# Kernel optimization log

Measured on AMD Instinct MI355X. Metric: run time of the kernel, lower is better.

## Reference

```python
import jax, jax.numpy as jnp
import numpy as np

HEADS = 8
DIM_HEAD = 64
QUERY_DIM = 1024
CONTEXT_DIM = 768
INNER = HEADS * DIM_HEAD  # 512


def setup_inputs() -> dict:
    key = jax.random.key(0)
    ks = jax.random.split(key, 8)
    b, n, j = 4, 2048, 2048
    x = jax.random.normal(ks[0], (b, n, QUERY_DIM), dtype=jnp.float32)
    context = jax.random.normal(ks[1], (b, j, CONTEXT_DIM), dtype=jnp.float32)
    mask = jax.random.randint(ks[2], (b, j), 0, 2).astype(jnp.bool_)
    # weights stored as (in, out) so forward is x @ W (torch Linear stores transpose)
    W_q = jax.random.normal(ks[3], (QUERY_DIM, INNER), dtype=jnp.float32) / np.sqrt(QUERY_DIM)
    W_k = jax.random.normal(ks[4], (CONTEXT_DIM, INNER), dtype=jnp.float32) / np.sqrt(CONTEXT_DIM)
    W_v = jax.random.normal(ks[5], (CONTEXT_DIM, INNER), dtype=jnp.float32) / np.sqrt(CONTEXT_DIM)
    W_o = jax.random.normal(ks[6], (INNER, QUERY_DIM), dtype=jnp.float32) / np.sqrt(INNER)
    b_o = jax.random.normal(ks[7], (QUERY_DIM,), dtype=jnp.float32) * 0.01
    return {"x": x, "context": context, "mask": mask,
            "W_q": W_q, "W_k": W_k, "W_v": W_v, "W_o": W_o, "b_o": b_o}


def reference(x, context, mask, W_q, W_k, W_v, W_o, b_o):
    b, n, _ = x.shape
    j = context.shape[1]
    scale = DIM_HEAD ** -0.5
    # projections -> [b, n, h, d]
    q = (x @ W_q).reshape(b, n, HEADS, DIM_HEAD)
    k = (context @ W_k).reshape(b, j, HEADS, DIM_HEAD)
    v = (context @ W_v).reshape(b, j, HEADS, DIM_HEAD)
    # similarity [b, h, n, j]
    sim = jnp.einsum('bihd,bjhd->bhij', q, k) * scale
    max_neg = -jnp.finfo(sim.dtype).max
    sim = jnp.where(mask[:, None, None, :], sim, max_neg)
    attn = jax.nn.softmax(sim, axis=-1)
    out = jnp.einsum('bhij,bjhd->bihd', attn, v).reshape(b, n, INNER)
    return out @ W_o + b_o  # dropout is identity (p=0 / eval)
```

## Files before the change

kernel.cpp:

```cpp
#include <hip/hip_runtime.h>
#include <hip/hip_bf16.h>

typedef __attribute__((ext_vector_type(4)))  float  f32x4;
typedef __attribute__((ext_vector_type(16))) float  f32x16;
typedef __attribute__((ext_vector_type(8)))  short  bf16x8;
typedef __attribute__((ext_vector_type(4)))  int    int32x4;
typedef __attribute__((ext_vector_type(2)))  unsigned int uint32x2;

#define DEVINL static __device__ __forceinline__
#define GAS __attribute__((address_space(1)))
#define LAS __attribute__((address_space(3)))

DEVINL ushort f2bf(float f) {
  unsigned u = __builtin_bit_cast(unsigned, f);
  unsigned r = u + 0x7fffu + ((u >> 16) & 1u);
  return (ushort)(r >> 16);
}

DEVINL unsigned cvtpk(float lo, float hi) {
  unsigned r;
  asm("v_cvt_pk_bf16_f32 %0, %1, %2" : "=v"(r) : "v"(lo), "v"(hi));
  return r;
}

DEVINL void plswap(unsigned &a, unsigned &b) {
  asm("v_permlane32_swap_b32 %0, %1" : "+v"(a), "+v"(b));
}

DEVINL float fexp2(float x) { return __builtin_amdgcn_exp2f(x); }

DEVINL float bf2f(short s) {
  return __builtin_bit_cast(float, ((unsigned)(ushort)s) << 16);
}

DEVINL f32x4 mfma16(bf16x8 a, bf16x8 b, f32x4 c) {
  return __builtin_amdgcn_mfma_f32_16x16x32_bf16(a, b, c, 0, 0, 0);
}
DEVINL f32x16 mfma32(bf16x8 a, bf16x8 b, f32x16 c) {
  return __builtin_amdgcn_mfma_f32_32x32x16_bf16(a, b, c, 0, 0, 0);
}

__global__ __launch_bounds__(256)
void prep_k(const int* __restrict__ msk, float* __restrict__ mbias,
            const float* __restrict__ Wq, const float* __restrict__ Wk,
            const float* __restrict__ Wv, const float* __restrict__ Wo,
            ushort* __restrict__ WqT, ushort* __restrict__ WkT,
            ushort* __restrict__ WvT, ushort* __restrict__ WoT)
{
  __shared__ ushort Ts[64][72];
  int id = blockIdx.x;
  if (id >= 448) {
    int tid = (id - 448) * 256 + threadIdx.x;
    if (tid < 8192) mbias[tid] = msk[tid] ? 0.f : -1e30f;
    return;
  }
  const float* src; ushort* dst; int Kd, Nd, lid;
  if (id < 128)      { src = Wq; dst = WqT; Kd = 1024; Nd = 512;  lid = id; }
  else if (id < 224) { src = Wk; dst = WkT; Kd = 768;  Nd = 512;  lid = id - 128; }
  else if (id < 320) { src = Wv; dst = WvT; Kd = 768;  Nd = 512;  lid = id - 224; }
  else               { src = Wo; dst = WoT; Kd = 512;  Nd = 1024; lid = id - 320; }
  const int sh = (Nd == 512) ? 3 : 4;
  const int kb = lid >> sh, nb = lid & ((1 << sh) - 1);
  const int k0 = kb * 64, n0 = nb * 64;
  const int t = threadIdx.x;
  const int r = t >> 2, c0 = (t & 3) * 16;

  const float* sp = src + (size_t)(k0 + r) * Nd + n0 + c0;
  f32x4 v0 = *(const f32x4*)(sp);
  f32x4 v1 = *(const f32x4*)(sp + 4);
  f32x4 v2 = *(const f32x4*)(sp + 8);
  f32x4 v3 = *(const f32x4*)(sp + 12);
  #pragma unroll
  for (int e = 0; e < 4; e++) {
    Ts[c0 + e][r]      = f2bf(v0[e]);
    Ts[c0 + 4 + e][r]  = f2bf(v1[e]);
    Ts[c0 + 8 + e][r]  = f2bf(v2[e]);
    Ts[c0 + 12 + e][r] = f2bf(v3[e]);
  }
  __syncthreads();
  const int n = t >> 2, kc = (t & 3) * 16;
  bf16x8 o0 = *(const bf16x8*)&Ts[n][kc];
  bf16x8 o1 = *(const bf16x8*)&Ts[n][kc + 8];
  ushort* dp = dst + (size_t)(n0 + n) * Kd + k0 + kc;
  *(bf16x8*)dp       = o0;
  *(bf16x8*)(dp + 8) = o1;
}

template<int PHASE>
__global__ __launch_bounds__(256)
void mm_k(const float* __restrict__ xf, const float* __restrict__ cf,
          const ushort* __restrict__ WqT, const ushort* __restrict__ WkT,
          const ushort* __restrict__ WvT,
          ushort* __restrict__ Qb, ushort* __restrict__ Kb, ushort* __restrict__ VT,
          const ushort* __restrict__ AO, const ushort* __restrict__ WoT,
          float* __restrict__ out, const float* __restrict__ bias)
{
  constexpr int AST = (PHASE == 0) ? 40 : 32;
  __shared__ ushort As[2][128 * AST];
  __shared__ ushort Bs[2][128 * 32];

  const float* Af = nullptr; const ushort* Ab = nullptr; const ushort* BT;
  ushort* Cw = nullptr;
  int Kd, mode, m0, n0;
  if (PHASE == 0) {
    int id = blockIdx.x;
    id = (id & 7) * 96 + (id >> 3);
    const int which = id >> 8, local = id & 255;
    m0 = (local >> 2) * 128; n0 = (local & 3) * 128;
    if (which == 0)      { Af = xf; BT = WqT; Cw = Qb; Kd = 1024; mode = 1; }
    else if (which == 1) { Af = cf; BT = WkT; Cw = Kb; Kd = 768;  mode = 1; }
    else                 { Af = cf; BT = WvT; Cw = VT; Kd = 768;  mode = 2; }
  } else {
    int id = blockIdx.x;
    id = (id & 7) * 64 + (id >> 3);
    m0 = (id >> 3) * 128; n0 = (id & 7) * 128;
    Ab = AO; BT = WoT; Kd = 512; mode = 0;
  }

  const int t = threadIdx.x, lane = t & 63, w = t >> 6;
  const int wr = w >> 1, wc = w & 1;
  const int g = lane >> 4, ql = lane & 15;

  const int arow = t >> 1, akc = (t & 1) * 16;
  const int srowo = 16 * w + (lane >> 2);
  const int sgg = (lane & 3) ^ ((lane >> 3) & 3);

  f32x4 acc[4][4];
  #pragma unroll
  for (int i = 0; i < 4; i++)
    #pragma unroll
    for (int j = 0; j < 4; j++) acc[i][j] = (f32x4){0.f, 0.f, 0.f, 0.f};

  auto stageB = [&](int buf, int k0) {
    #pragma unroll
    for (int i = 0; i < 2; i++) {
      const int row = i * 64 + srowo;
      const ushort* bsrc = BT + (size_t)(n0 + row) * Kd + k0 + sgg * 8;
      __builtin_amdgcn_global_load_lds((const GAS void*)bsrc,
          (LAS void*)&Bs[buf][(i * 64 + 16 * w) * 32], 16, 0, 0);
    }
  };
  auto stageA_lds = [&](int buf, int k0) {
    #pragma unroll
    for (int i = 0; i < 2; i++) {
      const int row = i * 64 + srowo;
      const ushort* asrc = Ab + (size_t)(m0 + row) * Kd + k0 + sgg * 8;
      __builtin_amdgcn_global_load_lds((const GAS void*)asrc,
          (LAS void*)&As[buf][(i * 64 + 16 * w) * 32], 16, 0, 0);
    }
  };
  auto writeA_f32 = [&](int buf, const f32x4& v0, const f32x4& v1,
                        const f32x4& v2, const f32x4& v3) {
    union { unsigned u[4]; int32x4 v; } w1_, w2_;
    w1_.u[0] = cvtpk(v0[0], v0[1]); w1_.u[1] = cvtpk(v0[2], v0[3]);
    w1_.u[2] = cvtpk(v1[0], v1[1]); w1_.u[3] = cvtpk(v1[2], v1[3]);
    w2_.u[0] = cvtpk(v2[0], v2[1]); w2_.u[1] = cvtpk(v2[2], v2[3]);
    w2_.u[2] = cvtpk(v3[0], v3[1]); w2_.u[3] = cvtpk(v3[2], v3[3]);
    ushort* dst = &As[buf][arow * 40 + akc];
    *(int32x4*)dst       = w1_.v;
    *(int32x4*)(dst + 8) = w2_.v;
  };

  const int NK = Kd >> 5;
  if (PHASE == 0) {
    const float* ap = Af + (size_t)(m0 + arow) * Kd + akc;
    f32x4 v0 = *(const f32x4*)(ap);
    f32x4 v1 = *(const f32x4*)(ap + 4);
    f32x4 v2 = *(const f32x4*)(ap + 8);
    f32x4 v3 = *(const f32x4*)(ap + 12);
    writeA_f32(0, v0, v1, v2, v3);
    stageB(0, 0);
  } else {
    stageA_lds(0, 0);
    stageB(0, 0);
  }
  __syncthreads();

  const int sel = (ql >> 1) & 3;
  const int koff = (g ^ sel) * 8;

  for (int tt = 0; tt < NK; tt++) {
    const int cur = tt & 1;
    const bool pre = (tt + 1 < NK);

    f32x4 n0v, n1v, n2v, n3v;
    if (PHASE == 0) {
      if (pre) {
        const float* ap = Af + (size_t)(m0 + arow) * Kd + (tt + 1) * 32 + akc;
        n0v = *(const f32x4*)(ap);
        n1v = *(const f32x4*)(ap + 4);
        n2v = *(const f32x4*)(ap + 8);
        n3v = *(const f32x4*)(ap + 12);
        stageB(cur ^ 1, (tt + 1) * 32);
      }
    } else {
      if (pre) { stageA_lds(cur ^ 1, (tt + 1) * 32); stageB(cur ^ 1, (tt + 1) * 32); }
    }

    bf16x8 af[4], bfr[4];
    #pragma unroll
    for (int i = 0; i < 4; i++) {
      if (PHASE == 0)
        af[i] = *(const bf16x8*)&As[cur][(wr * 64 + i * 16 + ql) * 40 + g * 8];
      else
        af[i] = *(const bf16x8*)&As[cur][(wr * 64 + i * 16 + ql) * 32 + koff];
      bfr[i] = *(const bf16x8*)&Bs[cur][(wc * 64 + i * 16 + ql) * 32 + koff];
    }
    #pragma unroll
    for (int i = 0; i < 4; i++)
      #pragma unroll
      for (int j = 0; j < 4; j++)
        acc[i][j] = mfma16(af[i], bfr[j], acc[i][j]);

    if (PHASE == 0 && pre) writeA_f32(cur ^ 1, n0v, n1v, n2v, n3v);
    __syncthreads();
  }

  #pragma unroll
  for (int i = 0; i < 4; i++) {
    #pragma unroll
    for (int j = 0; j < 4; j++) {
      int col = n0 + wc * 64 + j * 16 + ql;
      #pragma unroll
      for (int r = 0; r < 4; r++) {
        int mrow = m0 + wr * 64 + i * 16 + g * 4 + r;
        float v = acc[i][j][r];
        if (PHASE == 1) {
          out[(size_t)mrow * 1024 + col] = v + bias[col];
        } else {
          int b = mrow >> 11, nn = mrow & 2047;
          int hh = col >> 6, dd = col & 63;
          size_t base = (size_t)(b * 8 + hh) * 131072;
          if (mode == 1) Cw[base + (size_t)nn * 64 + dd]   = f2bf(v);
          else           Cw[base + (size_t)dd * 2048 + nn] = f2bf(v);
        }
      }
    }
  }
}

__global__ __launch_bounds__(512)
void attn_k(const ushort* __restrict__ Qb, const ushort* __restrict__ Kb,
            const ushort* __restrict__ VT, const float* __restrict__ mb,
            ushort* __restrict__ Opart, float2* __restrict__ Ml)
{
  constexpr int CHUNK = 512, NT = CHUNK / 64;
  __shared__ ushort Ks[2][64 * 64];
  __shared__ ushort Vs[2][64 * 64];

  const int bh = blockIdx.x, b = bh >> 3;
  const int sp = blockIdx.z;
  const int jb = sp * CHUNK;
  const int t = threadIdx.x, lane = t & 63, w = t >> 6;
  const int l31 = lane & 31, hi = lane >> 5;
  const int q0 = blockIdx.y * 256 + w * 32;

  const ushort* Qh = Qb + (size_t)bh * 131072;
  const ushort* Kh = Kb + (size_t)bh * 131072;
  const ushort* Vh = VT + (size_t)bh * 131072;
  const float* mp = mb + b * 2048 + 4 * hi;

  const int srow = lane >> 3;
  const int soff = ((lane & 7) * 16) ^ ((srow & 7) << 4);

  auto stage = [&](int buf, int j0) {
    const char* kg = (const char*)Kh + ((size_t)(j0 + 8 * w + srow)) * 128 + soff;
    __builtin_amdgcn_global_load_lds((const GAS void*)kg,
        (LAS void*)&Ks[buf][8 * w * 64], 16, 0, 0);
    const char* vg = (const char*)Vh + ((size_t)(8 * w + srow)) * 4096 + (size_t)j0 * 2 + soff;
    __builtin_amdgcn_global_load_lds((const GAS void*)vg,
        (LAS void*)&Vs[buf][8 * w * 64], 16, 0, 0);
  };

  bf16x8 qf[4];
  #pragma unroll
  for (int kk = 0; kk < 4; kk++)
    qf[kk] = *(const bf16x8*)(Qh + (size_t)(q0 + l31) * 64 + kk * 16 + 8 * hi);

  union { unsigned u[4]; bf16x8 v; } ones;
  ones.u[0] = 0x3F803F80u; ones.u[1] = 0x3F803F80u;
  ones.u[2] = 0x3F803F80u; ones.u[3] = 0x3F803F80u;

  f32x16 o0 = {}, o1 = {};
  float m = -1e30f, lsum = 0.f;
  const float sc = 0.18033688011112042f;

  stage(0, jb);
  __syncthreads();

  for (int tt = 0; tt < NT; ++tt) {
    const int cur = tt & 1;
    if (tt + 1 < NT) stage(cur ^ 1, jb + (tt + 1) * 64);

    #pragma unroll
    for (int js = 0; js < 2; ++js) {
      const int jloc = js * 32;
      const int j0 = jb + tt * 64 + jloc;

      f32x4 mb0 = *(const f32x4*)(mp + j0);
      f32x4 mb1 = *(const f32x4*)(mp + j0 + 8);
      f32x4 mb2 = *(const f32x4*)(mp + j0 + 16);
      f32x4 mb3 = *(const f32x4*)(mp + j0 + 24);

      const int krow = jloc + l31;
      const unsigned rsw = (unsigned)((l31 & 7) << 4);
      const char* kbase = (const char*)&Ks[cur][0] + krow * 128;
      bf16x8 kf0 = *(const bf16x8*)(kbase + ((0  + hi * 16) ^ rsw));
      bf16x8 kf1 = *(const bf16x8*)(kbase + ((32 + hi * 16) ^ rsw));
      bf16x8 kf2 = *(const bf16x8*)(kbase + ((64 + hi * 16) ^ rsw));
      bf16x8 kf3 = *(const bf16x8*)(kbase + ((96 + hi * 16) ^ rsw));

      __builtin_amdgcn_s_setprio(1);
      f32x16 z = {};
      f32x16 s = mfma32(kf0, qf[0], z);
      s = mfma32(kf1, qf[1], s);
      s = mfma32(kf2, qf[2], s);
      s = mfma32(kf3, qf[3], s);
      __builtin_amdgcn_s_setprio(0);

      const char* vb0 = (const char*)&Vs[cur][0] + l31 * 128;
      const char* vb1 = vb0 + 32 * 128;
      const unsigned vc0 = (unsigned)((jloc * 2 + hi * 16) ^ rsw);
      const unsigned vc1 = (unsigned)((jloc * 2 + 32 + hi * 16) ^ rsw);
      bf16x8 vf00 = *(const bf16x8*)(vb0 + vc0);
      bf16x8 vf01 = *(const bf16x8*)(vb0 + vc1);
      bf16x8 vf10 = *(const bf16x8*)(vb1 + vc0);
      bf16x8 vf11 = *(const bf16x8*)(vb1 + vc1);

      float pv[16];
      #pragma unroll
      for (int e = 0; e < 4; e++) {
        pv[e]      = fmaf(s[e],      sc, mb0[e]);
        pv[4 + e]  = fmaf(s[4 + e],  sc, mb1[e]);
        pv[8 + e]  = fmaf(s[8 + e],  sc, mb2[e]);
        pv[12 + e] = fmaf(s[12 + e], sc, mb3[e]);
      }

      float t0 = fmaxf(fmaxf(pv[0],  pv[1]),  pv[2]);
      float t1 = fmaxf(fmaxf(pv[3],  pv[4]),  pv[5]);
      float t2 = fmaxf(fmaxf(pv[6],  pv[7]),  pv[8]);
      float t3 = fmaxf(fmaxf(pv[9],  pv[10]), pv[11]);
      float t4 = fmaxf(fmaxf(pv[12], pv[13]), pv[14]);
      float pm = fmaxf(fmaxf(fmaxf(t0, t1), t2), fmaxf(fmaxf(t3, t4), pv[15]));
      pm = fmaxf(pm, __shfl_xor(pm, 32));

      if (!__all(pm <= m + 8.f)) {
        float mn = fmaxf(m, pm);
        float al = fexp2(m - mn);
        lsum *= al;
        #pragma unroll
        for (int r = 0; r < 16; r++) { o0[r] *= al; o1[r] *= al; }
        m = mn;
      }

      #pragma unroll
      for (int r = 0; r < 16; r++) pv[r] = fexp2(pv[r] - m);

      unsigned pk01 = cvtpk(pv[0],  pv[1]),  pk23 = cvtpk(pv[2],  pv[3]);
      unsigned pk45 = cvtpk(pv[4],  pv[5]),  pk67 = cvtpk(pv[6],  pv[7]);
      unsigned pk89 = cvtpk(pv[8],  pv[9]),  pkAB = cvtpk(pv[10], pv[11]);
      unsigned pkCD = cvtpk(pv[12], pv[13]), pkEF = cvtpk(pv[14], pv[15]);
      plswap(pk01, pk45);
      plswap(pk23, pk67);
      plswap(pk89, pkCD);
      plswap(pkAB, pkEF);
      union { unsigned u[4]; bf16x8 v; } pf0, pf1;
      pf0.u[0] = pk01; pf0.u[1] = pk23; pf0.u[2] = pk45; pf0.u[3] = pk67;
      pf1.u[0] = pk89; pf1.u[1] = pkAB; pf1.u[2] = pkCD; pf1.u[3] = pkEF;

      __builtin_amdgcn_s_setprio(1);
      f32x16 zs = {};
      zs = mfma32(ones.v, pf0.v, zs);
      zs = mfma32(ones.v, pf1.v, zs);
      o0 = mfma32(vf00, pf0.v, o0);
      o0 = mfma32(vf01, pf1.v, o0);
      o1 = mfma32(vf10, pf0.v, o1);
      o1 = mfma32(vf11, pf1.v, o1);
      __builtin_amdgcn_s_setprio(0);
      lsum += zs[0];
    }
    __syncthreads();
  }

  float inv = lsum > 0.f ? 1.0f / lsum : 0.f;
  const int q = q0 + l31;
  ushort* op = Opart + (size_t)sp * 4194304 + ((size_t)(bh * 2048 + q)) * 64;
  #pragma unroll
  for (int grp = 0; grp < 4; grp++) {
    int d0 = grp * 8 + 4 * hi;
    uint32x2 w0, w1;
    w0[0] = cvtpk(o0[4 * grp] * inv, o0[4 * grp + 1] * inv);
    w0[1] = cvtpk(o0[4 * grp + 2] * inv, o0[4 * grp + 3] * inv);
    w1[0] = cvtpk(o1[4 * grp] * inv, o1[4 * grp + 1] * inv);
    w1[1] = cvtpk(o1[4 * grp + 2] * inv, o1[4 * grp + 3] * inv);
    *(uint32x2*)(op + d0)      = w0;
    *(uint32x2*)(op + 32 + d0) = w1;
  }
  if (hi == 0) {
    float2 v; v.x = m; v.y = lsum;
    Ml[sp * 65536 + bh * 2048 + q] = v;
  }
}

__global__ __launch_bounds__(256)
void reduce_k(const ushort* __restrict__ Opart, const float2* __restrict__ Ml,
              ushort* __restrict__ AO)
{
  const int idx = blockIdx.x * 256 + threadIdx.x;
  const int d8 = idx & 7, q = (idx >> 3) & 2047, bh = idx >> 14;
  const int b = bh >> 3, h = bh & 7;

  float2 ml[4];
  float M = -1e30f;
  #pragma unroll
  for (int s = 0; s < 4; s++) {
    ml[s] = Ml[s * 65536 + bh * 2048 + q];
    M = fmaxf(M, ml[s].x);
  }
  float wgt[4], L = 0.f;
  #pragma unroll
  for (int s = 0; s < 4; s++) {
    wgt[s] = ml[s].y * fexp2(ml[s].x - M);
    L += wgt[s];
  }
  float invL = 1.f / L;

  float acc[8] = {0.f,0.f,0.f,0.f,0.f,0.f,0.f,0.f};
  #pragma unroll
  for (int s = 0; s < 4; s++) {
    bf16x8 v = *(const bf16x8*)(Opart + (size_t)s * 4194304 +
                                ((size_t)(bh * 2048 + q)) * 64 + d8 * 8);
    float ws = wgt[s] * invL;
    #pragma unroll
    for (int e = 0; e < 8; e++) acc[e] += ws * bf2f(v[e]);
  }

  union { unsigned u[4]; int32x4 v; } pk;
  pk.u[0] = cvtpk(acc[0], acc[1]);
  pk.u[1] = cvtpk(acc[2], acc[3]);
  pk.u[2] = cvtpk(acc[4], acc[5]);
  pk.u[3] = cvtpk(acc[6], acc[7]);
  *(int32x4*)(AO + ((size_t)(b * 2048 + q)) * 512 + h * 64 + d8 * 8) = pk.v;
}

extern "C" void kernel_launch(void* const* d_in, const int* in_sizes, int n_in,
                              void* d_out, int out_size, void* d_ws, size_t ws_size,
                              hipStream_t stream)
{
  const float* x   = (const float*)d_in[0];
  const float* ctx = (const float*)d_in[1];
  const int*   mk  = (const int*)d_in[2];
  const float* Wq  = (const float*)d_in[3];
  const float* Wk  = (const float*)d_in[4];
  const float* Wv  = (const float*)d_in[5];
  const float* Wo  = (const float*)d_in[6];
  const float* bo  = (const float*)d_in[7];
  float* out = (float*)d_out;

  ushort* Qb  = (ushort*)d_ws;
  ushort* Kb  = Qb + 4194304;
  ushort* VT  = Kb + 4194304;
  ushort* WoT = VT + 4194304;
  float*  mb  = (float*)(WoT + 524288);
  ushort* R2  = WoT + 524288 + 16384;
  ushort* WqT = R2;
  ushort* WkT = WqT + 524288;
  ushort* WvT = WkT + 393216;
  ushort* Opart = WvT + 393216;
  float2* Ml    = (float2*)(Opart + 16777216);
  ushort* AO    = Qb;

  prep_k<<<480, 256, 0, stream>>>(mk, mb, Wq, Wk, Wv, Wo, WqT, WkT, WvT, WoT);
  mm_k<0><<<768, 256, 0, stream>>>(x, ctx, WqT, WkT, WvT, Qb, Kb, VT,
                                   nullptr, nullptr, nullptr, nullptr);
  attn_k<<<dim3(32, 8, 4), 512, 0, stream>>>(Qb, Kb, VT, mb, Opart, Ml);
  reduce_k<<<2048, 256, 0, stream>>>(Opart, Ml, AO);
  mm_k<1><<<512, 256, 0, stream>>>(nullptr, nullptr, nullptr, nullptr, nullptr,
                                   nullptr, nullptr, nullptr, AO, WoT, out, bo);
}
```

Measured before the change: 143.0 us.

## Prefetch fp32 A tiles two iterations ahead with explicit waitcnt in projection GEMM

For the fp32-input projection phase, the GEMM loop now keeps two register buffers of A data and issues the global loads two K-steps ahead, while B is staged to LDS one step ahead. It uses sched_barriers and a manual s_waitcnt vmcnt(4) so the in-flight A prefetch does not force a full drain before each barrier. The goal is to hide global load latency behind the MFMA block. The cost is higher register pressure from the extra 16 floats per thread, and the hand-written wait counts are fragile.

```diff
diff --git a/kernel.cpp b/kernel.cpp
--- a/kernel.cpp
+++ b/kernel.cpp
@@ -149,54 +149,29 @@
           (LAS void*)&As[buf][(i * 64 + 16 * w) * 32], 16, 0, 0);
     }
   };
-  auto writeA_f32 = [&](int buf, const f32x4& v0, const f32x4& v1,
-                        const f32x4& v2, const f32x4& v3) {
-    union { unsigned u[4]; int32x4 v; } w1_, w2_;
-    w1_.u[0] = cvtpk(v0[0], v0[1]); w1_.u[1] = cvtpk(v0[2], v0[3]);
-    w1_.u[2] = cvtpk(v1[0], v1[1]); w1_.u[3] = cvtpk(v1[2], v1[3]);
-    w2_.u[0] = cvtpk(v2[0], v2[1]); w2_.u[1] = cvtpk(v2[2], v2[3]);
-    w2_.u[2] = cvtpk(v3[0], v3[1]); w2_.u[3] = cvtpk(v3[2], v3[3]);
-    ushort* dst = &As[buf][arow * 40 + akc];
-    *(int32x4*)dst       = w1_.v;
-    *(int32x4*)(dst + 8) = w2_.v;
-  };
-
-  const int NK = Kd >> 5;
-  if (PHASE == 0) {
-    const float* ap = Af + (size_t)(m0 + arow) * Kd + akc;
-    f32x4 v0 = *(const f32x4*)(ap);
-    f32x4 v1 = *(const f32x4*)(ap + 4);
-    f32x4 v2 = *(const f32x4*)(ap + 8);
-    f32x4 v3 = *(const f32x4*)(ap + 12);
-    writeA_f32(0, v0, v1, v2, v3);
-    stageB(0, 0);
-  } else {
-    stageA_lds(0, 0);
-    stageB(0, 0);
-  }
-  __syncthreads();
+  auto loadA_f32 = [&](int k0, f32x4 (&d)[4]) {
+    const float* ap = Af + (size_t)(m0 + arow) * Kd + k0 + akc;
+    d[0] = *(const f32x4*)(ap);
+    d[1] = *(const f32x4*)(ap + 4);
+    d[2] = *(const f32x4*)(ap + 8);
+    d[3] = *(const f32x4*)(ap + 12);
+  };
+  auto writeA_f32 = [&](int buf, const f32x4 (&v)[4]) {
+    union { unsigned u[4]; int32x4 vv; } w1_, w2_;
+    w1_.u[0] = cvtpk(v[0][0], v[0][1]); w1_.u[1] = cvtpk(v[0][2], v[0][3]);
+    w1_.u[2] = cvtpk(v[1][0], v[1][1]); w1_.u[3] = cvtpk(v[1][2], v[1][3]);
+    w2_.u[0] = cvtpk(v[2][0], v[2][1]); w2_.u[1] = cvtpk(v[2][2], v[2][3]);
+    w2_.u[2] = cvtpk(v[3][0], v[3][1]); w2_.u[3] = cvtpk(v[3][2], v[3][3]);
+    ushort* dst = &As[0][0] + (size_t)buf * 128 * 40 + arow * 40 + akc;
+    *(int32x4*)dst       = w1_.vv;
+    *(int32x4*)(dst + 8) = w2_.vv;
+  };
 
   const int sel = (ql >> 1) & 3;
   const int koff = (g ^ sel) * 8;
-
-  for (int tt = 0; tt < NK; tt++) {
-    const int cur = tt & 1;
-    const bool pre = (tt + 1 < NK);
-
-    f32x4 n0v, n1v, n2v, n3v;
-    if (PHASE == 0) {
-      if (pre) {
-        const float* ap = Af + (size_t)(m0 + arow) * Kd + (tt + 1) * 32 + akc;
-        n0v = *(const f32x4*)(ap);
-        n1v = *(const f32x4*)(ap + 4);
-        n2v = *(const f32x4*)(ap + 8);
-        n3v = *(const f32x4*)(ap + 12);
-        stageB(cur ^ 1, (tt + 1) * 32);
-      }
-    } else {
-      if (pre) { stageA_lds(cur ^ 1, (tt + 1) * 32); stageB(cur ^ 1, (tt + 1) * 32); }
-    }
-
+  const int NK = Kd >> 5;
+
+  auto mfmaBlock = [&](int cur) {
     bf16x8 af[4], bfr[4];
     #pragma unroll
     for (int i = 0; i < 4; i++) {
@@ -211,9 +186,44 @@
       #pragma unroll
       for (int j = 0; j < 4; j++)
         acc[i][j] = mfma16(af[i], bfr[j], acc[i][j]);
-
-    if (PHASE == 0 && pre) writeA_f32(cur ^ 1, n0v, n1v, n2v, n3v);
+  };
+
+  if (PHASE == 0) {
+    f32x4 pS0[4], pS1[4];
+    loadA_f32(0, pS0);
+    writeA_f32(0, pS0);
+    stageB(0, 0);
+    loadA_f32(32, pS0);
     __syncthreads();
+
+    auto bodyP0 = [&](int tt, int cur, f32x4 (&consume)[4], f32x4 (&fill)[4]) {
+      const bool nb = (tt + 1 < NK);
+      const bool nl = (tt + 2 < NK);
+      if (nb) stageB(cur ^ 1, (tt + 1) * 32);
+      __builtin_amdgcn_sched_barrier(0);
+      if (nl) loadA_f32((tt + 2) * 32, fill);
+      __builtin_amdgcn_sched_barrier(0);
+      mfmaBlock(cur);
+      if (nb) writeA_f32(cur ^ 1, consume);
+      if (nl) asm volatile("s_waitcnt vmcnt(4) lgkmcnt(0)" ::: "memory");
+      else    asm volatile("s_waitcnt vmcnt(0) lgkmcnt(0)" ::: "memory");
+      __builtin_amdgcn_s_barrier();
+      __builtin_amdgcn_sched_barrier(0);
+    };
+    for (int tt = 0; tt < NK; tt += 2) {
+      bodyP0(tt,     0, pS0, pS1);
+      bodyP0(tt + 1, 1, pS1, pS0);
+    }
+  } else {
+    stageA_lds(0, 0);
+    stageB(0, 0);
+    __syncthreads();
+    for (int tt = 0; tt < NK; tt++) {
+      const int cur = tt & 1;
+      if (tt + 1 < NK) { stageA_lds(cur ^ 1, (tt + 1) * 32); stageB(cur ^ 1, (tt + 1) * 32); }
+      mfmaBlock(cur);
+      __syncthreads();
+    }
   }
 
   #pragma unroll
```

Result: no change. 141.4 us (median of 5 runs) (-1.1%).
